# Kernel tuning notes

Measured on AMD Instinct MI355X. Metric: run time of the kernel, lower is better.

The kernel has to match this reference:

```python
import jax, jax.numpy as jnp
import numpy as np

N_NODES = 50000
N_EDGES = 800000
D_IN = 128
D_HID = 128
D_OUT = 128


def _sage_conv(x, edge_index, Wp, bp, Wl, bl, Wr):
    """PyG SAGEConv with project=True, mean aggregation, root weight, bias.

    x: [N, d_in]; edge_index: [2, E] (row 0 = src j, row 1 = dst i).
    out = mean_j relu(x_j @ Wp.T + bp) @ Wl.T + bl + x_i @ Wr.T
    """
    src, dst = edge_index[0], edge_index[1]
    n = x.shape[0]
    h = jax.nn.relu(x @ Wp.T + bp)          # [N, d_in] projected neighbor feats
    msg = h[src]                             # [E, d_in] gather
    agg_sum = jax.ops.segment_sum(msg, dst, num_segments=n)          # [N, d_in]
    cnt = jax.ops.segment_sum(jnp.ones((msg.shape[0],), x.dtype), dst,
                              num_segments=n)                        # [N]
    agg = agg_sum / jnp.maximum(cnt, 1.0)[:, None]                   # mean
    return agg @ Wl.T + bl + x @ Wr.T


def setup_inputs() -> dict:
    key = jax.random.key(0)
    ks = jax.random.split(key, 12)
    s = lambda d: 1.0 / np.sqrt(d)
    x = jax.random.normal(ks[0], (N_NODES, D_IN), dtype=jnp.float32)
    edge_index = jax.random.randint(ks[1], (2, N_EDGES), 0, N_NODES, dtype=jnp.int64)
    return {
        "x": x,
        "edge_index": edge_index,
        # layer 1
        "Wp1": jax.random.normal(ks[2], (D_IN, D_IN), jnp.float32) * s(D_IN),
        "bp1": jnp.zeros((D_IN,), jnp.float32),
        "Wl1": jax.random.normal(ks[3], (D_HID, D_IN), jnp.float32) * s(D_IN),
        "bl1": jnp.zeros((D_HID,), jnp.float32),
        "Wr1": jax.random.normal(ks[4], (D_HID, D_IN), jnp.float32) * s(D_IN),
        # layer 2
        "Wp2": jax.random.normal(ks[5], (D_HID, D_HID), jnp.float32) * s(D_HID),
        "bp2": jnp.zeros((D_HID,), jnp.float32),
        "Wl2": jax.random.normal(ks[6], (D_OUT, D_HID), jnp.float32) * s(D_HID),
        "bl2": jnp.zeros((D_OUT,), jnp.float32),
        "Wr2": jax.random.normal(ks[7], (D_OUT, D_HID), jnp.float32) * s(D_HID),
    }


def reference(x, edge_index, Wp1, bp1, Wl1, bl1, Wr1, Wp2, bp2, Wl2, bl2, Wr2):
    h = jax.nn.relu(_sage_conv(x, edge_index, Wp1, bp1, Wl1, bl1, Wr1))
    out = _sage_conv(h, edge_index, Wp2, bp2, Wl2, bl2, Wr2)
    return out
```

## Files before the change

### kernel.cpp

```cpp
#include <hip/hip_runtime.h>

#define NN 50000
#define NE 800000
#define D 128
#define NTILE 3128
#define GGRID 768
#define XBLK 6250
#define WBLK 96
#define BBLK 250
#define EPB 3200
#define NBUCK 196
#define STAGE_CAP 64
#define BIN_CAP 4608
#define SORT_WIN 4608
#define LDS_STRIDE 136

typedef __attribute__((ext_vector_type(8))) short bf16x8;
typedef __attribute__((ext_vector_type(4))) float f32x4;

__device__ inline unsigned short f2bf(float f) {
    union { float f; unsigned u; } v; v.f = f;
    unsigned r = v.u + 0x7FFF + ((v.u >> 16) & 1);
    return (unsigned short)(r >> 16);
}
__device__ inline float bf2f(unsigned b) {
    union { unsigned u; float f; } v; v.u = b << 16;
    return v.f;
}

__global__ __launch_bounds__(256)
void prep(const float* __restrict__ x,
          const float* __restrict__ w0, const float* __restrict__ w1,
          const float* __restrict__ w2, const float* __restrict__ w3,
          const float* __restrict__ w4, const float* __restrict__ w5,
          const int* __restrict__ ei,
          unsigned short* __restrict__ xb, unsigned short* __restrict__ wb,
          unsigned* __restrict__ bin, int* __restrict__ bcur) {
    const unsigned b = blockIdx.x;
    if (b < XBLK) {
        int i = b * 256 + threadIdx.x;
        float4 v = ((const float4*)x)[i];
        ushort4 o = {f2bf(v.x), f2bf(v.y), f2bf(v.z), f2bf(v.w)};
        ((ushort4*)xb)[i] = o;
    } else if (b < XBLK + WBLK) {
        const float* ws_[6] = {w0, w1, w2, w3, w4, w5};
        int wi = (int)(b - XBLK) >> 4;
        int off = ((int)(b - XBLK) & 15) * 256 + threadIdx.x;
        float4 v = ((const float4*)ws_[wi])[off];
        ushort4 o = {f2bf(v.x), f2bf(v.y), f2bf(v.z), f2bf(v.w)};
        ((ushort4*)(wb + wi * D * D))[off] = o;
    } else {
        __shared__ unsigned stage[NBUCK * STAGE_CAP];
        __shared__ int bcnt[NBUCK];
        __shared__ int sbase[NBUCK];
        const int ebase = (int)(b - XBLK - WBLK) * EPB;
        if (threadIdx.x < NBUCK) bcnt[threadIdx.x] = 0;
        __syncthreads();
        for (int j = threadIdx.x; j < EPB; j += 256) {
            const int e = ebase + j;
            const int dst = ei[NE + e];
            const int src = ei[e];
            const int bk = dst >> 8;
            const unsigned u = (unsigned)src | ((unsigned)(dst & 255) << 16);
            const int slot = atomicAdd(&bcnt[bk], 1);
            if (slot < STAGE_CAP) {
                stage[bk * STAGE_CAP + slot] = u;
            } else {
                const int gp = atomicAdd(&bcur[bk], 1);
                if (gp < BIN_CAP) bin[bk * BIN_CAP + gp] = u;
            }
        }
        __syncthreads();
        if (threadIdx.x < NBUCK) {
            int c = bcnt[threadIdx.x];
            if (c > STAGE_CAP) c = STAGE_CAP;
            sbase[threadIdx.x] = atomicAdd(&bcur[threadIdx.x], c);
        }
        __syncthreads();
        const int wv = threadIdx.x >> 6, ln = threadIdx.x & 63;
        for (int bk = wv; bk < NBUCK; bk += 4) {
            int c = bcnt[bk];
            if (c > STAGE_CAP) c = STAGE_CAP;
            if (ln < c) {
                int p = sbase[bk] + ln;
                if (p < BIN_CAP) bin[bk * BIN_CAP + p] = stage[bk * STAGE_CAP + ln];
            }
        }
    }
}

__global__ __launch_bounds__(256)
void bucket_scan(const int* __restrict__ bcur, int* __restrict__ bbase,
                 int* __restrict__ row_start) {
    __shared__ int tmp[256];
    int v = (threadIdx.x < NBUCK) ? bcur[threadIdx.x] : 0;
    tmp[threadIdx.x] = v;
    __syncthreads();
    for (int off = 1; off < 256; off <<= 1) {
        int t = (threadIdx.x >= (unsigned)off) ? tmp[threadIdx.x - off] : 0;
        __syncthreads();
        tmp[threadIdx.x] += t;
        __syncthreads();
    }
    if (threadIdx.x <= NBUCK)
        bbase[threadIdx.x] = (threadIdx.x == 0) ? 0 : tmp[threadIdx.x - 1];
    if (threadIdx.x == 0) row_start[NN] = NE;
}

template <typename OUTT, bool DUAL>
__device__ inline void gemm_body(const unsigned short* __restrict__ A1,
                                 const unsigned short* __restrict__ W1,
                                 const unsigned short* __restrict__ A2,
                                 const unsigned short* __restrict__ W2,
                                 const float* __restrict__ bias,
                                 OUTT* __restrict__ out, int do_relu,
                                 int bid, int nblk) {
    const int lane = threadIdx.x & 63;
    const int wave = threadIdx.x >> 6;
    const int quad = lane >> 4;
    const int l16 = lane & 15;
    const int c0 = wave * 32 + l16;
    const int c1 = c0 + 16;

    const float bv0 = bias[c0];
    const float bv1 = bias[c1];

    bf16x8 w10[4], w11[4], w20[4], w21[4];
#pragma unroll
    for (int kt = 0; kt < 4; ++kt) {
        const int ko = kt * 32 + quad * 8;
        w10[kt] = *(const bf16x8*)&W1[c0 * D + ko];
        w11[kt] = *(const bf16x8*)&W1[c1 * D + ko];
        if (DUAL) {
            w20[kt] = *(const bf16x8*)&W2[c0 * D + ko];
            w21[kt] = *(const bf16x8*)&W2[c1 * D + ko];
        }
    }

    for (int t = bid; t < NTILE; t += nblk) {
        const int row0 = t * 16;
        int r = row0 + l16;
        const int arow = (r < NN ? r : NN - 1) * D;

        f32x4 acc0 = (f32x4){0.f, 0.f, 0.f, 0.f};
        f32x4 acc1 = (f32x4){0.f, 0.f, 0.f, 0.f};
#pragma unroll
        for (int kt = 0; kt < 4; ++kt) {
            const int ko = kt * 32 + quad * 8;
            bf16x8 a1 = *(const bf16x8*)&A1[arow + ko];
            acc0 = __builtin_amdgcn_mfma_f32_16x16x32_bf16(a1, w10[kt], acc0, 0, 0, 0);
            acc1 = __builtin_amdgcn_mfma_f32_16x16x32_bf16(a1, w11[kt], acc1, 0, 0, 0);
            if (DUAL) {
                bf16x8 a2 = *(const bf16x8*)&A2[arow + ko];
                acc0 = __builtin_amdgcn_mfma_f32_16x16x32_bf16(a2, w20[kt], acc0, 0, 0, 0);
                acc1 = __builtin_amdgcn_mfma_f32_16x16x32_bf16(a2, w21[kt], acc1, 0, 0, 0);
            }
        }

#pragma unroll
        for (int rr = 0; rr < 4; ++rr) {
            const int row = row0 + quad * 4 + rr;
            if (row < NN) {
                float v0 = acc0[rr] + bv0;
                float v1 = acc1[rr] + bv1;
                if (do_relu) {
                    v0 = v0 > 0.f ? v0 : 0.f;
                    v1 = v1 > 0.f ? v1 : 0.f;
                }
                if constexpr (sizeof(OUTT) == 2) {
                    out[row * D + c0] = (OUTT)f2bf(v0);
                    out[row * D + c1] = (OUTT)f2bf(v1);
                } else {
                    out[row * D + c0] = (OUTT)v0;
                    out[row * D + c1] = (OUTT)v1;
                }
            }
        }
    }
}

template <typename OUTT, bool DUAL>
__global__ __launch_bounds__(256)
void gemm_persist(const unsigned short* __restrict__ A1,
                  const unsigned short* __restrict__ W1,
                  const unsigned short* __restrict__ A2,
                  const unsigned short* __restrict__ W2,
                  const float* __restrict__ bias, OUTT* __restrict__ out,
                  int do_relu) {
    gemm_body<OUTT, DUAL>(A1, W1, A2, W2, bias, out, do_relu, blockIdx.x, GGRID);
}

__global__ __launch_bounds__(256)
void combine_proj(const unsigned short* __restrict__ Ag,
                  const unsigned short* __restrict__ Wl,
                  const unsigned short* __restrict__ X,
                  const unsigned short* __restrict__ Wr,
                  const float* __restrict__ bl, unsigned short* __restrict__ bufH,
                  const unsigned short* __restrict__ Wp,
                  const float* __restrict__ bp, unsigned short* __restrict__ bufP2) {
    __shared__ unsigned short tile[16 * LDS_STRIDE];
    const int lane = threadIdx.x & 63;
    const int wave = threadIdx.x >> 6;
    const int quad = lane >> 4;
    const int l16 = lane & 15;
    const int c0 = wave * 32 + l16;
    const int c1 = c0 + 16;

    const float bl0 = bl[c0], bl1 = bl[c1];
    const float bp0 = bp[c0], bp1 = bp[c1];

    bf16x8 wl0[4], wl1[4], wr0[4], wr1[4];
#pragma unroll
    for (int kt = 0; kt < 4; ++kt) {
        const int ko = kt * 32 + quad * 8;
        wl0[kt] = *(const bf16x8*)&Wl[c0 * D + ko];
        wl1[kt] = *(const bf16x8*)&Wl[c1 * D + ko];
        wr0[kt] = *(const bf16x8*)&Wr[c0 * D + ko];
        wr1[kt] = *(const bf16x8*)&Wr[c1 * D + ko];
    }

    for (int t = blockIdx.x; t < NTILE; t += GGRID) {
        const int row0 = t * 16;
        int r = row0 + l16;
        const int arow = (r < NN ? r : NN - 1) * D;

        f32x4 acc0 = (f32x4){0.f, 0.f, 0.f, 0.f};
        f32x4 acc1 = (f32x4){0.f, 0.f, 0.f, 0.f};
#pragma unroll
        for (int kt = 0; kt < 4; ++kt) {
            const int ko = kt * 32 + quad * 8;
            bf16x8 a1 = *(const bf16x8*)&Ag[arow + ko];
            bf16x8 a2 = *(const bf16x8*)&X[arow + ko];
            acc0 = __builtin_amdgcn_mfma_f32_16x16x32_bf16(a1, wl0[kt], acc0, 0, 0, 0);
            acc1 = __builtin_amdgcn_mfma_f32_16x16x32_bf16(a1, wl1[kt], acc1, 0, 0, 0);
            acc0 = __builtin_amdgcn_mfma_f32_16x16x32_bf16(a2, wr0[kt], acc0, 0, 0, 0);
            acc1 = __builtin_amdgcn_mfma_f32_16x16x32_bf16(a2, wr1[kt], acc1, 0, 0, 0);
        }
#pragma unroll
        for (int rr = 0; rr < 4; ++rr) {
            const int row = row0 + quad * 4 + rr;
            float v0 = acc0[rr] + bl0;
            float v1 = acc1[rr] + bl1;
            v0 = v0 > 0.f ? v0 : 0.f;
            v1 = v1 > 0.f ? v1 : 0.f;
            const unsigned short h0 = f2bf(v0), h1 = f2bf(v1);
            tile[(quad * 4 + rr) * LDS_STRIDE + c0] = h0;
            tile[(quad * 4 + rr) * LDS_STRIDE + c1] = h1;
            if (row < NN) {
                bufH[row * D + c0] = h0;
                bufH[row * D + c1] = h1;
            }
        }
        __syncthreads();

        f32x4 p0 = (f32x4){0.f, 0.f, 0.f, 0.f};
        f32x4 p1 = (f32x4){0.f, 0.f, 0.f, 0.f};
#pragma unroll
        for (int kt = 0; kt < 4; ++kt) {
            const int ko = kt * 32 + quad * 8;
            bf16x8 aL = *(const bf16x8*)&tile[l16 * LDS_STRIDE + ko];
            bf16x8 wp0 = *(const bf16x8*)&Wp[c0 * D + ko];
            bf16x8 wp1 = *(const bf16x8*)&Wp[c1 * D + ko];
            p0 = __builtin_amdgcn_mfma_f32_16x16x32_bf16(aL, wp0, p0, 0, 0, 0);
            p1 = __builtin_amdgcn_mfma_f32_16x16x32_bf16(aL, wp1, p1, 0, 0, 0);
        }
#pragma unroll
        for (int rr = 0; rr < 4; ++rr) {
            const int row = row0 + quad * 4 + rr;
            if (row < NN) {
                float v0 = p0[rr] + bp0;
                float v1 = p1[rr] + bp1;
                v0 = v0 > 0.f ? v0 : 0.f;
                v1 = v1 > 0.f ? v1 : 0.f;
                bufP2[row * D + c0] = f2bf(v0);
                bufP2[row * D + c1] = f2bf(v1);
            }
        }
        __syncthreads();
    }
}

__global__ __launch_bounds__(256)
void gemm_fill(const unsigned short* __restrict__ A,
               const unsigned short* __restrict__ W,
               const float* __restrict__ bias, unsigned short* __restrict__ outp,
               const int* __restrict__ bbase, const unsigned* __restrict__ bin,
               int* __restrict__ row_start, unsigned short* __restrict__ src16) {
    if (blockIdx.x < GGRID) {
        gemm_body<unsigned short, false>(A, W, nullptr, nullptr, bias, outp, 1,
                                         blockIdx.x, GGRID);
        return;
    }
    __shared__ int hist[256];
    __shared__ unsigned short win[SORT_WIN];
    const int b = (int)blockIdx.x - GGRID;
    const int nbase = b << 8;
    const int nn = (NN - nbase < 256) ? (NN - nbase) : 256;
    const int gb = bbase[b];
    const int span = bbase[b + 1] - gb;
    const unsigned* mybin = bin + (size_t)b * BIN_CAP;

    hist[threadIdx.x] = 0;
    __syncthreads();
    for (int i = threadIdx.x; i < span; i += 256)
        atomicAdd(&hist[mybin[i] >> 16], 1);
    __syncthreads();

    const int hv = hist[threadIdx.x];
    __syncthreads();
    hist[threadIdx.x] = hv;
    __syncthreads();
    for (int off = 1; off < 256; off <<= 1) {
        int tv = (threadIdx.x >= (unsigned)off) ? hist[threadIdx.x - off] : 0;
        __syncthreads();
        hist[threadIdx.x] += tv;
        __syncthreads();
    }
    const int ex = hist[threadIdx.x] - hv;
    __syncthreads();
    hist[threadIdx.x] = ex;
    if ((int)threadIdx.x < nn) row_start[nbase + threadIdx.x] = gb + ex;
    __syncthreads();

    for (int i = threadIdx.x; i < span; i += 256) {
        const unsigned u = mybin[i];
        const int pos = atomicAdd(&hist[u >> 16], 1);
        const unsigned short sv = (unsigned short)(u & 0xffffu);
        if (pos < SORT_WIN) win[pos] = sv;
        else src16[gb + pos] = sv;
    }
    __syncthreads();
    const int lim = span < SORT_WIN ? span : SORT_WIN;
    for (int i = threadIdx.x; i < lim; i += 256) src16[gb + i] = win[i];
}

__device__ inline void acc8(float* s, uint4 r) {
    s[0] += bf2f(r.x & 0xffffu); s[1] += bf2f(r.x >> 16);
    s[2] += bf2f(r.y & 0xffffu); s[3] += bf2f(r.y >> 16);
    s[4] += bf2f(r.z & 0xffffu); s[5] += bf2f(r.z >> 16);
    s[6] += bf2f(r.w & 0xffffu); s[7] += bf2f(r.w >> 16);
}

__global__ __launch_bounds__(256)
void gather_mean4(const uint4* __restrict__ P4, const int* __restrict__ row_start,
                  const unsigned short* __restrict__ src16,
                  uint4* __restrict__ agg4) {
    const int n = blockIdx.x * 4 + (threadIdx.x >> 6);
    const int lane = threadIdx.x & 63;
    const int q = lane >> 4;
    const int l16 = lane & 15;
    const int b = row_start[n];
    const int e = row_start[n + 1];

    float s[8];
#pragma unroll
    for (int j = 0; j < 8; ++j) s[j] = 0.f;

    int i = b;
    for (; i + 32 <= e; i += 32) {
        int idx[8];
        uint4 r[8];
#pragma unroll
        for (int j = 0; j < 8; ++j) idx[j] = src16[i + j * 4 + q];
#pragma unroll
        for (int j = 0; j < 8; ++j) r[j] = P4[idx[j] * 16 + l16];
#pragma unroll
        for (int j = 0; j < 8; ++j) acc8(s, r[j]);
    }
    for (; i + 16 <= e; i += 16) {
        int i0 = src16[i + 0 + q], i1 = src16[i + 4 + q];
        int i2 = src16[i + 8 + q], i3 = src16[i + 12 + q];
        uint4 r0 = P4[i0 * 16 + l16];
        uint4 r1 = P4[i1 * 16 + l16];
        uint4 r2 = P4[i2 * 16 + l16];
        uint4 r3 = P4[i3 * 16 + l16];
        acc8(s, r0); acc8(s, r1); acc8(s, r2); acc8(s, r3);
    }
    for (; i + 4 <= e; i += 4) {
        int i0 = src16[i + q];
        uint4 r0 = P4[i0 * 16 + l16];
        acc8(s, r0);
    }
    const int rem = e - i;
    if (q < rem) {
        int i0 = src16[i + q];
        uint4 r0 = P4[i0 * 16 + l16];
        acc8(s, r0);
    }

#pragma unroll
    for (int j = 0; j < 8; ++j) {
        s[j] += __shfl_xor(s[j], 16);
        s[j] += __shfl_xor(s[j], 32);
    }

    const int deg = e - b;
    const float inv = 1.0f / (float)(deg > 0 ? deg : 1);
    if (q == 0) {
        uint4 o;
        o.x = (unsigned)f2bf(s[0] * inv) | ((unsigned)f2bf(s[1] * inv) << 16);
        o.y = (unsigned)f2bf(s[2] * inv) | ((unsigned)f2bf(s[3] * inv) << 16);
        o.z = (unsigned)f2bf(s[4] * inv) | ((unsigned)f2bf(s[5] * inv) << 16);
        o.w = (unsigned)f2bf(s[6] * inv) | ((unsigned)f2bf(s[7] * inv) << 16);
        agg4[n * 16 + l16] = o;
    }
}

extern "C" void kernel_launch(void* const* d_in, const int* in_sizes, int n_in,
                              void* d_out, int out_size, void* d_ws, size_t ws_size,
                              hipStream_t stream) {
    const float* x   = (const float*)d_in[0];
    const int*   ei  = (const int*)d_in[1];
    const float* Wp1 = (const float*)d_in[2];
    const float* bp1 = (const float*)d_in[3];
    const float* Wl1 = (const float*)d_in[4];
    const float* bl1 = (const float*)d_in[5];
    const float* Wr1 = (const float*)d_in[6];
    const float* Wp2 = (const float*)d_in[7];
    const float* bp2 = (const float*)d_in[8];
    const float* Wl2 = (const float*)d_in[9];
    const float* bl2 = (const float*)d_in[10];
    const float* Wr2 = (const float*)d_in[11];
    float* out = (float*)d_out;

    char* ws = (char*)d_ws;
    size_t off = 0;
    auto alloc = [&](size_t bytes) {
        void* p = ws + off;
        off += (bytes + 511) & ~511ull;
        return p;
    };
    unsigned short* Wb   = (unsigned short*)alloc((size_t)6 * D * D * 2);
    unsigned short* xb   = (unsigned short*)alloc((size_t)NN * D * 2);
    unsigned short* bufP = (unsigned short*)alloc((size_t)NN * D * 2);
    unsigned short* bufAg= (unsigned short*)alloc((size_t)NN * D * 2);
    unsigned short* bufH = (unsigned short*)alloc((size_t)NN * D * 2);
    int* row_start  = (int*)alloc((size_t)(NN + 1) * 4);
    int* bcur       = (int*)alloc((size_t)NBUCK * 4);
    int* bbase      = (int*)alloc((size_t)(NBUCK + 1) * 4);
    unsigned* bin   = (unsigned*)alloc((size_t)NBUCK * BIN_CAP * 4);
    unsigned short* src16 = (unsigned short*)alloc((size_t)NE * 2);

    hipMemsetAsync(bcur, 0, (size_t)NBUCK * 4, stream);
    prep<<<XBLK + WBLK + BBLK, 256, 0, stream>>>(
        x, Wp1, Wl1, Wr1, Wp2, Wl2, Wr2, ei, xb, Wb, bin, bcur);

    bucket_scan<<<1, 256, 0, stream>>>(bcur, bbase, row_start);

    gemm_fill<<<GGRID + NBUCK, 256, 0, stream>>>(
        xb, Wb + 0 * D * D, bp1, bufP, bbase, bin, row_start, src16);

    const int GA = NN / 4;

    gather_mean4<<<GA, 256, 0, stream>>>(
        (const uint4*)bufP, row_start, src16, (uint4*)bufAg);
    combine_proj<<<GGRID, 256, 0, stream>>>(
        bufAg, Wb + 1 * D * D, xb, Wb + 2 * D * D, bl1, bufH,
        Wb + 3 * D * D, bp2, bufP);

    gather_mean4<<<GA, 256, 0, stream>>>(
        (const uint4*)bufP, row_start, src16, (uint4*)bufAg);
    gemm_persist<float, true><<<GGRID, 256, 0, stream>>>(
        bufAg, Wb + 4 * D * D, bufH, Wb + 5 * D * D, bl2, out, 0);
}
```

Before: 248.8 us.

## Fuse neighbor mean-gather into the combine/projection GEMM kernels via LDS tiles

Replaces the separate gather_mean4 kernels and the persistent combine GEMMs with two fused kernels. In each, a block of four waves gathers and averages 16 destination rows into an LDS tile, then immediately runs the MFMA combine (and, for layer 1, the next projection) on that tile. This removes the bf16 aggregate write and read-back through global memory and drops two kernel launches. In exchange, each block reloads weights from global or cache per 16-row tile instead of keeping them in registers across a persistent loop, and the grid becomes one block per tile. Uneven node degrees may also cause imbalance between waves inside a block.

```diff
diff --git a/kernel.cpp b/kernel.cpp
--- a/kernel.cpp
+++ b/kernel.cpp
@@ -107,13 +107,10 @@
     if (threadIdx.x == 0) row_start[NN] = NE;
 }
 
-template <typename OUTT, bool DUAL>
-__device__ inline void gemm_body(const unsigned short* __restrict__ A1,
-                                 const unsigned short* __restrict__ W1,
-                                 const unsigned short* __restrict__ A2,
-                                 const unsigned short* __restrict__ W2,
+__device__ inline void gemm_body(const unsigned short* __restrict__ A,
+                                 const unsigned short* __restrict__ W,
                                  const float* __restrict__ bias,
-                                 OUTT* __restrict__ out, int do_relu,
+                                 unsigned short* __restrict__ out,
                                  int bid, int nblk) {
     const int lane = threadIdx.x & 63;
     const int wave = threadIdx.x >> 6;
@@ -125,16 +122,12 @@
     const float bv0 = bias[c0];
     const float bv1 = bias[c1];
 
-    bf16x8 w10[4], w11[4], w20[4], w21[4];
+    bf16x8 w10[4], w11[4];
 #pragma unroll
     for (int kt = 0; kt < 4; ++kt) {
         const int ko = kt * 32 + quad * 8;
-        w10[kt] = *(const bf16x8*)&W1[c0 * D + ko];
-        w11[kt] = *(const bf16x8*)&W1[c1 * D + ko];
-        if (DUAL) {
-            w20[kt] = *(const bf16x8*)&W2[c0 * D + ko];
-            w21[kt] = *(const bf16x8*)&W2[c1 * D + ko];
-        }
+        w10[kt] = *(const bf16x8*)&W[c0 * D + ko];
+        w11[kt] = *(const bf16x8*)&W[c1 * D + ko];
     }
 
     for (int t = bid; t < NTILE; t += nblk) {
@@ -147,14 +140,9 @@
 #pragma unroll
         for (int kt = 0; kt < 4; ++kt) {
             const int ko = kt * 32 + quad * 8;
-            bf16x8 a1 = *(const bf16x8*)&A1[arow + ko];
+            bf16x8 a1 = *(const bf16x8*)&A[arow + ko];
             acc0 = __builtin_amdgcn_mfma_f32_16x16x32_bf16(a1, w10[kt], acc0, 0, 0, 0);
             acc1 = __builtin_amdgcn_mfma_f32_16x16x32_bf16(a1, w11[kt], acc1, 0, 0, 0);
-            if (DUAL) {
-                bf16x8 a2 = *(const bf16x8*)&A2[arow + ko];
-                acc0 = __builtin_amdgcn_mfma_f32_16x16x32_bf16(a2, w20[kt], acc0, 0, 0, 0);
-                acc1 = __builtin_amdgcn_mfma_f32_16x16x32_bf16(a2, w21[kt], acc1, 0, 0, 0);
-            }
         }
 
 #pragma unroll
@@ -163,120 +151,12 @@
             if (row < NN) {
                 float v0 = acc0[rr] + bv0;
                 float v1 = acc1[rr] + bv1;
-                if (do_relu) {
-                    v0 = v0 > 0.f ? v0 : 0.f;
-                    v1 = v1 > 0.f ? v1 : 0.f;
-                }
-                if constexpr (sizeof(OUTT) == 2) {
-                    out[row * D + c0] = (OUTT)f2bf(v0);
-                    out[row * D + c1] = (OUTT)f2bf(v1);
-                } else {
-                    out[row * D + c0] = (OUTT)v0;
-                    out[row * D + c1] = (OUTT)v1;
-                }
-            }
-        }
-    }
-}
-
-template <typename OUTT, bool DUAL>
-__global__ __launch_bounds__(256)
-void gemm_persist(const unsigned short* __restrict__ A1,
-                  const unsigned short* __restrict__ W1,
-                  const unsigned short* __restrict__ A2,
-                  const unsigned short* __restrict__ W2,
-                  const float* __restrict__ bias, OUTT* __restrict__ out,
-                  int do_relu) {
-    gemm_body<OUTT, DUAL>(A1, W1, A2, W2, bias, out, do_relu, blockIdx.x, GGRID);
-}
-
-__global__ __launch_bounds__(256)
-void combine_proj(const unsigned short* __restrict__ Ag,
-                  const unsigned short* __restrict__ Wl,
-                  const unsigned short* __restrict__ X,
-                  const unsigned short* __restrict__ Wr,
-                  const float* __restrict__ bl, unsigned short* __restrict__ bufH,
-                  const unsigned short* __restrict__ Wp,
-                  const float* __restrict__ bp, unsigned short* __restrict__ bufP2) {
-    __shared__ unsigned short tile[16 * LDS_STRIDE];
-    const int lane = threadIdx.x & 63;
-    const int wave = threadIdx.x >> 6;
-    const int quad = lane >> 4;
-    const int l16 = lane & 15;
-    const int c0 = wave * 32 + l16;
-    const int c1 = c0 + 16;
-
-    const float bl0 = bl[c0], bl1 = bl[c1];
-    const float bp0 = bp[c0], bp1 = bp[c1];
-
-    bf16x8 wl0[4], wl1[4], wr0[4], wr1[4];
-#pragma unroll
-    for (int kt = 0; kt < 4; ++kt) {
-        const int ko = kt * 32 + quad * 8;
-        wl0[kt] = *(const bf16x8*)&Wl[c0 * D + ko];
-        wl1[kt] = *(const bf16x8*)&Wl[c1 * D + ko];
-        wr0[kt] = *(const bf16x8*)&Wr[c0 * D + ko];
-        wr1[kt] = *(const bf16x8*)&Wr[c1 * D + ko];
-    }
-
-    for (int t = blockIdx.x; t < NTILE; t += GGRID) {
-        const int row0 = t * 16;
-        int r = row0 + l16;
-        const int arow = (r < NN ? r : NN - 1) * D;
-
-        f32x4 acc0 = (f32x4){0.f, 0.f, 0.f, 0.f};
-        f32x4 acc1 = (f32x4){0.f, 0.f, 0.f, 0.f};
-#pragma unroll
-        for (int kt = 0; kt < 4; ++kt) {
-            const int ko = kt * 32 + quad * 8;
-            bf16x8 a1 = *(const bf16x8*)&Ag[arow + ko];
-            bf16x8 a2 = *(const bf16x8*)&X[arow + ko];
-            acc0 = __builtin_amdgcn_mfma_f32_16x16x32_bf16(a1, wl0[kt], acc0, 0, 0, 0);
-            acc1 = __builtin_amdgcn_mfma_f32_16x16x32_bf16(a1, wl1[kt], acc1, 0, 0, 0);
-            acc0 = __builtin_amdgcn_mfma_f32_16x16x32_bf16(a2, wr0[kt], acc0, 0, 0, 0);
-            acc1 = __builtin_amdgcn_mfma_f32_16x16x32_bf16(a2, wr1[kt], acc1, 0, 0, 0);
-        }
-#pragma unroll
-        for (int rr = 0; rr < 4; ++rr) {
-            const int row = row0 + quad * 4 + rr;
-            float v0 = acc0[rr] + bl0;
-            float v1 = acc1[rr] + bl1;
-            v0 = v0 > 0.f ? v0 : 0.f;
-            v1 = v1 > 0.f ? v1 : 0.f;
-            const unsigned short h0 = f2bf(v0), h1 = f2bf(v1);
-            tile[(quad * 4 + rr) * LDS_STRIDE + c0] = h0;
-            tile[(quad * 4 + rr) * LDS_STRIDE + c1] = h1;
-            if (row < NN) {
-                bufH[row * D + c0] = h0;
-                bufH[row * D + c1] = h1;
-            }
-        }
-        __syncthreads();
-
-        f32x4 p0 = (f32x4){0.f, 0.f, 0.f, 0.f};
-        f32x4 p1 = (f32x4){0.f, 0.f, 0.f, 0.f};
-#pragma unroll
-        for (int kt = 0; kt < 4; ++kt) {
-            const int ko = kt * 32 + quad * 8;
-            bf16x8 aL = *(const bf16x8*)&tile[l16 * LDS_STRIDE + ko];
-            bf16x8 wp0 = *(const bf16x8*)&Wp[c0 * D + ko];
-            bf16x8 wp1 = *(const bf16x8*)&Wp[c1 * D + ko];
-            p0 = __builtin_amdgcn_mfma_f32_16x16x32_bf16(aL, wp0, p0, 0, 0, 0);
-            p1 = __builtin_amdgcn_mfma_f32_16x16x32_bf16(aL, wp1, p1, 0, 0, 0);
-        }
-#pragma unroll
-        for (int rr = 0; rr < 4; ++rr) {
-            const int row = row0 + quad * 4 + rr;
-            if (row < NN) {
-                float v0 = p0[rr] + bp0;
-                float v1 = p1[rr] + bp1;
                 v0 = v0 > 0.f ? v0 : 0.f;
                 v1 = v1 > 0.f ? v1 : 0.f;
-                bufP2[row * D + c0] = f2bf(v0);
-                bufP2[row * D + c1] = f2bf(v1);
+                out[row * D + c0] = f2bf(v0);
+                out[row * D + c1] = f2bf(v1);
             }
         }
-        __syncthreads();
     }
 }
 
@@ -287,8 +167,7 @@
                const int* __restrict__ bbase, const unsigned* __restrict__ bin,
                int* __restrict__ row_start, unsigned short* __restrict__ src16) {
     if (blockIdx.x < GGRID) {
-        gemm_body<unsigned short, false>(A, W, nullptr, nullptr, bias, outp, 1,
-                                         blockIdx.x, GGRID);
+        gemm_body(A, W, bias, outp, blockIdx.x, GGRID);
         return;
     }
     __shared__ int hist[256];
@@ -341,68 +220,214 @@
     s[6] += bf2f(r.w & 0xffffu); s[7] += bf2f(r.w >> 16);
 }
 
-__global__ __launch_bounds__(256)
-void gather_mean4(const uint4* __restrict__ P4, const int* __restrict__ row_start,
-                  const unsigned short* __restrict__ src16,
-                  uint4* __restrict__ agg4) {
-    const int n = blockIdx.x * 4 + (threadIdx.x >> 6);
+__device__ inline void gather_tile(const uint4* __restrict__ P4,
+                                   const int* __restrict__ row_start,
+                                   const unsigned short* __restrict__ src16,
+                                   int row0, unsigned short* tile) {
     const int lane = threadIdx.x & 63;
+    const int wave = threadIdx.x >> 6;
     const int q = lane >> 4;
     const int l16 = lane & 15;
-    const int b = row_start[n];
-    const int e = row_start[n + 1];
-
-    float s[8];
-#pragma unroll
-    for (int j = 0; j < 8; ++j) s[j] = 0.f;
-
-    int i = b;
-    for (; i + 32 <= e; i += 32) {
-        int idx[8];
-        uint4 r[8];
-#pragma unroll
-        for (int j = 0; j < 8; ++j) idx[j] = src16[i + j * 4 + q];
-#pragma unroll
-        for (int j = 0; j < 8; ++j) r[j] = P4[idx[j] * 16 + l16];
-#pragma unroll
-        for (int j = 0; j < 8; ++j) acc8(s, r[j]);
-    }
-    for (; i + 16 <= e; i += 16) {
-        int i0 = src16[i + 0 + q], i1 = src16[i + 4 + q];
-        int i2 = src16[i + 8 + q], i3 = src16[i + 12 + q];
-        uint4 r0 = P4[i0 * 16 + l16];
-        uint4 r1 = P4[i1 * 16 + l16];
-        uint4 r2 = P4[i2 * 16 + l16];
-        uint4 r3 = P4[i3 * 16 + l16];
-        acc8(s, r0); acc8(s, r1); acc8(s, r2); acc8(s, r3);
-    }
-    for (; i + 4 <= e; i += 4) {
-        int i0 = src16[i + q];
-        uint4 r0 = P4[i0 * 16 + l16];
-        acc8(s, r0);
-    }
-    const int rem = e - i;
-    if (q < rem) {
-        int i0 = src16[i + q];
-        uint4 r0 = P4[i0 * 16 + l16];
-        acc8(s, r0);
-    }
-
-#pragma unroll
-    for (int j = 0; j < 8; ++j) {
-        s[j] += __shfl_xor(s[j], 16);
-        s[j] += __shfl_xor(s[j], 32);
-    }
-
-    const int deg = e - b;
-    const float inv = 1.0f / (float)(deg > 0 ? deg : 1);
-    if (q == 0) {
-        uint4 o;
-        o.x = (unsigned)f2bf(s[0] * inv) | ((unsigned)f2bf(s[1] * inv) << 16);
-        o.y = (unsigned)f2bf(s[2] * inv) | ((unsigned)f2bf(s[3] * inv) << 16);
-        o.z = (unsigned)f2bf(s[4] * inv) | ((unsigned)f2bf(s[5] * inv) << 16);
-        o.w = (unsigned)f2bf(s[6] * inv) | ((unsigned)f2bf(s[7] * inv) << 16);
-        agg4[n * 16 + l16] = o;
+#pragma unroll
+    for (int j = 0; j < 4; ++j) {
+        const int rl = wave * 4 + j;
+        const int n = row0 + rl;
+        int b = 0, e = 0;
+        if (n < NN) { b = row_start[n]; e = row_start[n + 1]; }
+
+        float s[8];
+#pragma unroll
+        for (int k = 0; k < 8; ++k) s[k] = 0.f;
+
+        int i = b;
+        for (; i + 32 <= e; i += 32) {
+            int idx[8];
+            uint4 r[8];
+#pragma unroll
+            for (int k = 0; k < 8; ++k) idx[k] = src16[i + k * 4 + q];
+#pragma unroll
+            for (int k = 0; k < 8; ++k) r[k] = P4[idx[k] * 16 + l16];
+#pragma unroll
+            for (int k = 0; k < 8; ++k) acc8(s, r[k]);
+        }
+        for (; i + 16 <= e; i += 16) {
+            int i0 = src16[i + 0 + q], i1 = src16[i + 4 + q];
+            int i2 = src16[i + 8 + q], i3 = src16[i + 12 + q];
+            uint4 r0 = P4[i0 * 16 + l16];
+            uint4 r1 = P4[i1 * 16 + l16];
+            uint4 r2 = P4[i2 * 16 + l16];
+            uint4 r3 = P4[i3 * 16 + l16];
+            acc8(s, r0); acc8(s, r1); acc8(s, r2); acc8(s, r3);
+        }
+        for (; i + 4 <= e; i += 4) {
+            int i0 = src16[i + q];
+            uint4 r0 = P4[i0 * 16 + l16];
+            acc8(s, r0);
+        }
+        const int rem = e - i;
+        if (q < rem) {
+            int i0 = src16[i + q];
+            uint4 r0 = P4[i0 * 16 + l16];
+            acc8(s, r0);
+        }
+
+#pragma unroll
+        for (int k = 0; k < 8; ++k) {
+            s[k] += __shfl_xor(s[k], 16);
+            s[k] += __shfl_xor(s[k], 32);
+        }
+
+        const int deg = e - b;
+        const float inv = 1.0f / (float)(deg > 0 ? deg : 1);
+        if (q == 0) {
+            uint4 o;
+            o.x = (unsigned)f2bf(s[0] * inv) | ((unsigned)f2bf(s[1] * inv) << 16);
+            o.y = (unsigned)f2bf(s[2] * inv) | ((unsigned)f2bf(s[3] * inv) << 16);
+            o.z = (unsigned)f2bf(s[4] * inv) | ((unsigned)f2bf(s[5] * inv) << 16);
+            o.w = (unsigned)f2bf(s[6] * inv) | ((unsigned)f2bf(s[7] * inv) << 16);
+            *(uint4*)&tile[rl * LDS_STRIDE + l16 * 8] = o;
+        }
+    }
+}
+
+__global__ __launch_bounds__(256, 4)
+void gather_combine_proj(const uint4* __restrict__ P4,
+                         const int* __restrict__ row_start,
+                         const unsigned short* __restrict__ src16,
+                         const unsigned short* __restrict__ Wl,
+                         const unsigned short* __restrict__ X,
+                         const unsigned short* __restrict__ Wr,
+                         const float* __restrict__ bl,
+                         unsigned short* __restrict__ bufH,
+                         const unsigned short* __restrict__ Wp,
+                         const float* __restrict__ bp,
+                         unsigned short* __restrict__ bufP2) {
+    __shared__ __align__(16) unsigned short tile[16 * LDS_STRIDE];
+    const int lane = threadIdx.x & 63;
+    const int wave = threadIdx.x >> 6;
+    const int quad = lane >> 4;
+    const int l16 = lane & 15;
+    const int row0 = blockIdx.x * 16;
+
+    gather_tile(P4, row_start, src16, row0, tile);
+    __syncthreads();
+
+    const int c0 = wave * 32 + l16;
+    const int c1 = c0 + 16;
+    int r = row0 + l16;
+    const int arow = (r < NN ? r : NN - 1) * D;
+
+    f32x4 acc0 = (f32x4){0.f, 0.f, 0.f, 0.f};
+    f32x4 acc1 = (f32x4){0.f, 0.f, 0.f, 0.f};
+#pragma unroll
+    for (int kt = 0; kt < 4; ++kt) {
+        const int ko = kt * 32 + quad * 8;
+        bf16x8 aL = *(const bf16x8*)&tile[l16 * LDS_STRIDE + ko];
+        bf16x8 aX = *(const bf16x8*)&X[arow + ko];
+        bf16x8 bl0 = *(const bf16x8*)&Wl[c0 * D + ko];
+        bf16x8 bl1 = *(const bf16x8*)&Wl[c1 * D + ko];
+        bf16x8 br0 = *(const bf16x8*)&Wr[c0 * D + ko];
+        bf16x8 br1 = *(const bf16x8*)&Wr[c1 * D + ko];
+        acc0 = __builtin_amdgcn_mfma_f32_16x16x32_bf16(aL, bl0, acc0, 0, 0, 0);
+        acc1 = __builtin_amdgcn_mfma_f32_16x16x32_bf16(aL, bl1, acc1, 0, 0, 0);
+        acc0 = __builtin_amdgcn_mfma_f32_16x16x32_bf16(aX, br0, acc0, 0, 0, 0);
+        acc1 = __builtin_amdgcn_mfma_f32_16x16x32_bf16(aX, br1, acc1, 0, 0, 0);
+    }
+    __syncthreads();
+
+    const float b0 = bl[c0], b1 = bl[c1];
+#pragma unroll
+    for (int rr = 0; rr < 4; ++rr) {
+        const int row = row0 + quad * 4 + rr;
+        float v0 = acc0[rr] + b0;
+        float v1 = acc1[rr] + b1;
+        v0 = v0 > 0.f ? v0 : 0.f;
+        v1 = v1 > 0.f ? v1 : 0.f;
+        const unsigned short h0 = f2bf(v0), h1 = f2bf(v1);
+        tile[(quad * 4 + rr) * LDS_STRIDE + c0] = h0;
+        tile[(quad * 4 + rr) * LDS_STRIDE + c1] = h1;
+        if (row < NN) {
+            bufH[row * D + c0] = h0;
+            bufH[row * D + c1] = h1;
+        }
+    }
+    __syncthreads();
+
+    f32x4 p0 = (f32x4){0.f, 0.f, 0.f, 0.f};
+    f32x4 p1 = (f32x4){0.f, 0.f, 0.f, 0.f};
+#pragma unroll
+    for (int kt = 0; kt < 4; ++kt) {
+        const int ko = kt * 32 + quad * 8;
+        bf16x8 aL = *(const bf16x8*)&tile[l16 * LDS_STRIDE + ko];
+        bf16x8 wp0 = *(const bf16x8*)&Wp[c0 * D + ko];
+        bf16x8 wp1 = *(const bf16x8*)&Wp[c1 * D + ko];
+        p0 = __builtin_amdgcn_mfma_f32_16x16x32_bf16(aL, wp0, p0, 0, 0, 0);
+        p1 = __builtin_amdgcn_mfma_f32_16x16x32_bf16(aL, wp1, p1, 0, 0, 0);
+    }
+    const float q0 = bp[c0], q1 = bp[c1];
+#pragma unroll
+    for (int rr = 0; rr < 4; ++rr) {
+        const int row = row0 + quad * 4 + rr;
+        if (row < NN) {
+            float v0 = p0[rr] + q0;
+            float v1 = p1[rr] + q1;
+            v0 = v0 > 0.f ? v0 : 0.f;
+            v1 = v1 > 0.f ? v1 : 0.f;
+            bufP2[row * D + c0] = f2bf(v0);
+            bufP2[row * D + c1] = f2bf(v1);
+        }
+    }
+}
+
+__global__ __launch_bounds__(256, 4)
+void gather_combine_out(const uint4* __restrict__ P4,
+                        const int* __restrict__ row_start,
+                        const unsigned short* __restrict__ src16,
+                        const unsigned short* __restrict__ Wl,
+                        const unsigned short* __restrict__ H,
+                        const unsigned short* __restrict__ Wr,
+                        const float* __restrict__ bl,
+                        float* __restrict__ out) {
+    __shared__ __align__(16) unsigned short tile[16 * LDS_STRIDE];
+    const int lane = threadIdx.x & 63;
+    const int wave = threadIdx.x >> 6;
+    const int quad = lane >> 4;
+    const int l16 = lane & 15;
+    const int row0 = blockIdx.x * 16;
+
+    gather_tile(P4, row_start, src16, row0, tile);
+    __syncthreads();
+
+    const int c0 = wave * 32 + l16;
+    const int c1 = c0 + 16;
+    int r = row0 + l16;
+    const int arow = (r < NN ? r : NN - 1) * D;
+
+    f32x4 acc0 = (f32x4){0.f, 0.f, 0.f, 0.f};
+    f32x4 acc1 = (f32x4){0.f, 0.f, 0.f, 0.f};
+#pragma unroll
+    for (int kt = 0; kt < 4; ++kt) {
+        const int ko = kt * 32 + quad * 8;
+        bf16x8 aL = *(const bf16x8*)&tile[l16 * LDS_STRIDE + ko];
+        bf16x8 aH = *(const bf16x8*)&H[arow + ko];
+        bf16x8 bl0 = *(const bf16x8*)&Wl[c0 * D + ko];
+        bf16x8 bl1 = *(const bf16x8*)&Wl[c1 * D + ko];
+        bf16x8 br0 = *(const bf16x8*)&Wr[c0 * D + ko];
+        bf16x8 br1 = *(const bf16x8*)&Wr[c1 * D + ko];
+        acc0 = __builtin_amdgcn_mfma_f32_16x16x32_bf16(aL, bl0, acc0, 0, 0, 0);
+        acc1 = __builtin_amdgcn_mfma_f32_16x16x32_bf16(aL, bl1, acc1, 0, 0, 0);
+        acc0 = __builtin_amdgcn_mfma_f32_16x16x32_bf16(aH, br0, acc0, 0, 0, 0);
+        acc1 = __builtin_amdgcn_mfma_f32_16x16x32_bf16(aH, br1, acc1, 0, 0, 0);
+    }
+
+    const float b0 = bl[c0], b1 = bl[c1];
+#pragma unroll
+    for (int rr = 0; rr < 4; ++rr) {
+        const int row = row0 + quad * 4 + rr;
+        if (row < NN) {
+            out[row * D + c0] = acc0[rr] + b0;
+            out[row * D + c1] = acc1[rr] + b1;
+        }
     }
 }
 
@@ -433,7 +458,7 @@
     unsigned short* Wb   = (unsigned short*)alloc((size_t)6 * D * D * 2);
     unsigned short* xb   = (unsigned short*)alloc((size_t)NN * D * 2);
     unsigned short* bufP = (unsigned short*)alloc((size_t)NN * D * 2);
-    unsigned short* bufAg= (unsigned short*)alloc((size_t)NN * D * 2);
+    unsigned short* bufP2= (unsigned short*)alloc((size_t)NN * D * 2);
     unsigned short* bufH = (unsigned short*)alloc((size_t)NN * D * 2);
     int* row_start  = (int*)alloc((size_t)(NN + 1) * 4);
     int* bcur       = (int*)alloc((size_t)NBUCK * 4);
@@ -450,16 +475,12 @@
     gemm_fill<<<GGRID + NBUCK, 256, 0, stream>>>(
         xb, Wb + 0 * D * D, bp1, bufP, bbase, bin, row_start, src16);
 
-    const int GA = NN / 4;
-
-    gather_mean4<<<GA, 256, 0, stream>>>(
-        (const uint4*)bufP, row_start, src16, (uint4*)bufAg);
-    combine_proj<<<GGRID, 256, 0, stream>>>(
-        bufAg, Wb + 1 * D * D, xb, Wb + 2 * D * D, bl1, bufH,
-        Wb + 3 * D * D, bp2, bufP);
-
-    gather_mean4<<<GA, 256, 0, stream>>>(
-        (const uint4*)bufP, row_start, src16, (uint4*)bufAg);
-    gemm_persist<float, true><<<GGRID, 256, 0, stream>>>(
-        bufAg, Wb + 4 * D * D, bufH, Wb + 5 * D * D, bl2, out, 0);
-}
+    gather_combine_proj<<<NTILE, 256, 0, stream>>>(
+        (const uint4*)bufP, row_start, src16,
+        Wb + 1 * D * D, xb, Wb + 2 * D * D, bl1, bufH,
+        Wb + 3 * D * D, bp2, bufP2);
+
+    gather_combine_out<<<NTILE, 256, 0, stream>>>(
+        (const uint4*)bufP2, row_start, src16,
+        Wb + 4 * D * D, bufH, Wb + 5 * D * D, bl2, out);
+}
```

New measurement: 293.5 us. 18.0% more time.

## Fold bucket scan into gemm_fill, double GEMM grid, separate layer-2 projection buffer

Applied to the files above, without the earlier changes.

Removes the single-block bucket_scan launch. Each sorting block in gemm_fill now recomputes the bucket prefix sum itself from bcur, and the sorting blocks are placed first in the grid. GGRID doubles to 1536, which raises the block count of every persistent GEMM kernel. A new bufP2 buffer holds the layer-2 projection so combine_proj no longer overwrites bufP. The trade-off is one fewer kernel launch and more GEMM parallelism in exchange for a redundant per-block scan and more blocks sharing fixed work.

```diff
diff --git a/kernel.cpp b/kernel.cpp
--- a/kernel.cpp
+++ b/kernel.cpp
@@ -4,7 +4,7 @@
 #define NE 800000
 #define D 128
 #define NTILE 3128
-#define GGRID 768
+#define GGRID 1536
 #define XBLK 6250
 #define WBLK 96
 #define BBLK 250
@@ -89,24 +89,6 @@
     }
 }
 
-__global__ __launch_bounds__(256)
-void bucket_scan(const int* __restrict__ bcur, int* __restrict__ bbase,
-                 int* __restrict__ row_start) {
-    __shared__ int tmp[256];
-    int v = (threadIdx.x < NBUCK) ? bcur[threadIdx.x] : 0;
-    tmp[threadIdx.x] = v;
-    __syncthreads();
-    for (int off = 1; off < 256; off <<= 1) {
-        int t = (threadIdx.x >= (unsigned)off) ? tmp[threadIdx.x - off] : 0;
-        __syncthreads();
-        tmp[threadIdx.x] += t;
-        __syncthreads();
-    }
-    if (threadIdx.x <= NBUCK)
-        bbase[threadIdx.x] = (threadIdx.x == 0) ? 0 : tmp[threadIdx.x - 1];
-    if (threadIdx.x == 0) row_start[NN] = NE;
-}
-
 template <typename OUTT, bool DUAL>
 __device__ inline void gemm_body(const unsigned short* __restrict__ A1,
                                  const unsigned short* __restrict__ W1,
@@ -284,20 +266,32 @@
 void gemm_fill(const unsigned short* __restrict__ A,
                const unsigned short* __restrict__ W,
                const float* __restrict__ bias, unsigned short* __restrict__ outp,
-               const int* __restrict__ bbase, const unsigned* __restrict__ bin,
+               const int* __restrict__ bcur, const unsigned* __restrict__ bin,
                int* __restrict__ row_start, unsigned short* __restrict__ src16) {
-    if (blockIdx.x < GGRID) {
+    if (blockIdx.x >= NBUCK) {
         gemm_body<unsigned short, false>(A, W, nullptr, nullptr, bias, outp, 1,
-                                         blockIdx.x, GGRID);
+                                         (int)blockIdx.x - NBUCK, GGRID);
         return;
     }
     __shared__ int hist[256];
+    __shared__ int pref[256];
     __shared__ unsigned short win[SORT_WIN];
-    const int b = (int)blockIdx.x - GGRID;
+    const int b = (int)blockIdx.x;
     const int nbase = b << 8;
     const int nn = (NN - nbase < 256) ? (NN - nbase) : 256;
-    const int gb = bbase[b];
-    const int span = bbase[b + 1] - gb;
+
+    int v = (threadIdx.x < NBUCK) ? bcur[threadIdx.x] : 0;
+    pref[threadIdx.x] = v;
+    __syncthreads();
+    for (int off = 1; off < 256; off <<= 1) {
+        int t = (threadIdx.x >= (unsigned)off) ? pref[threadIdx.x - off] : 0;
+        __syncthreads();
+        pref[threadIdx.x] += t;
+        __syncthreads();
+    }
+    const int gb = (b == 0) ? 0 : pref[b - 1];
+    const int span = pref[b] - gb;
+    if (b == NBUCK - 1 && threadIdx.x == 0) row_start[NN] = NE;
     const unsigned* mybin = bin + (size_t)b * BIN_CAP;
 
     hist[threadIdx.x] = 0;
@@ -435,9 +429,9 @@
     unsigned short* bufP = (unsigned short*)alloc((size_t)NN * D * 2);
     unsigned short* bufAg= (unsigned short*)alloc((size_t)NN * D * 2);
     unsigned short* bufH = (unsigned short*)alloc((size_t)NN * D * 2);
+    unsigned short* bufP2= (unsigned short*)alloc((size_t)NN * D * 2);
     int* row_start  = (int*)alloc((size_t)(NN + 1) * 4);
     int* bcur       = (int*)alloc((size_t)NBUCK * 4);
-    int* bbase      = (int*)alloc((size_t)(NBUCK + 1) * 4);
     unsigned* bin   = (unsigned*)alloc((size_t)NBUCK * BIN_CAP * 4);
     unsigned short* src16 = (unsigned short*)alloc((size_t)NE * 2);
 
@@ -445,10 +439,8 @@
     prep<<<XBLK + WBLK + BBLK, 256, 0, stream>>>(
         x, Wp1, Wl1, Wr1, Wp2, Wl2, Wr2, ei, xb, Wb, bin, bcur);
 
-    bucket_scan<<<1, 256, 0, stream>>>(bcur, bbase, row_start);
-
-    gemm_fill<<<GGRID + NBUCK, 256, 0, stream>>>(
-        xb, Wb + 0 * D * D, bp1, bufP, bbase, bin, row_start, src16);
+    gemm_fill<<<NBUCK + GGRID, 256, 0, stream>>>(
+        xb, Wb + 0 * D * D, bp1, bufP, bcur, bin, row_start, src16);
 
     const int GA = NN / 4;
 
@@ -456,10 +448,10 @@
         (const uint4*)bufP, row_start, src16, (uint4*)bufAg);
     combine_proj<<<GGRID, 256, 0, stream>>>(
         bufAg, Wb + 1 * D * D, xb, Wb + 2 * D * D, bl1, bufH,
-        Wb + 3 * D * D, bp2, bufP);
+        Wb + 3 * D * D, bp2, bufP2);
 
     gather_mean4<<<GA, 256, 0, stream>>>(
-        (const uint4*)bufP, row_start, src16, (uint4*)bufAg);
+        (const uint4*)bufP2, row_start, src16, (uint4*)bufAg);
     gemm_persist<float, true><<<GGRID, 256, 0, stream>>>(
         bufAg, Wb + 4 * D * D, bufH, Wb + 5 * D * D, bl2, out, 0);
 }
```

New measurement: 263.1 us. +5.7%, slower.
